# Kernel tuning notes

Hardware: AMD Instinct MI355X
Metric: run time of the kernel (lower is better)

## Reference

```python
import jax, jax.numpy as jnp
import numpy as np

HIDDEN_NF = 256
ATOMICA_DIM = 512
NUM_HEADS = 4
HEAD_DIM = HIDDEN_NF // NUM_HEADS
EDGE_CUTOFF = 10.0
N_LIG = 1024
N_POCKET = 8192
BOX = 30.0  # Angstrom box so the cutoff mask is selective


def _lin(key, fan_in, fan_out):
    kw, kb = jax.random.split(key)
    s = 1.0 / np.sqrt(fan_in)
    W = jax.random.uniform(kw, (fan_in, fan_out), jnp.float32, -s, s)
    b = jax.random.uniform(kb, (fan_out,), jnp.float32, -s, s)
    return W, b


def setup_inputs() -> dict:
    key = jax.random.key(0)
    ks = jax.random.split(key, 12)
    h_lig = jax.random.normal(ks[0], (N_LIG, HIDDEN_NF), jnp.float32)
    x_lig = jax.random.uniform(ks[1], (N_LIG, 3), jnp.float32) * BOX
    h_atomica = jax.random.normal(ks[2], (N_POCKET, ATOMICA_DIM), jnp.float32)
    x_pocket = jax.random.uniform(ks[3], (N_POCKET, 3), jnp.float32) * BOX
    qw, qb = _lin(ks[4], HIDDEN_NF, HIDDEN_NF)
    kw, kb = _lin(ks[5], ATOMICA_DIM, HIDDEN_NF)
    vw, vb = _lin(ks[6], ATOMICA_DIM, HIDDEN_NF)
    ow, ob = _lin(ks[7], HIDDEN_NF, HIDDEN_NF)
    e1w, e1b = _lin(ks[8], 1, HIDDEN_NF)
    e2w, e2b = _lin(ks[9], HIDDEN_NF, NUM_HEADS)
    c1w, c1b = _lin(ks[10], HIDDEN_NF, HIDDEN_NF)
    c2w, c2b = _lin(ks[11], HIDDEN_NF, 1)
    return dict(h_lig=h_lig, x_lig=x_lig, h_atomica=h_atomica, x_pocket=x_pocket,
                qw=qw, qb=qb, kw=kw, kb=kb, vw=vw, vb=vb, ow=ow, ob=ob,
                e1w=e1w, e1b=e1b, e2w=e2w, e2b=e2b,
                c1w=c1w, c1b=c1b, c2w=c2w, c2b=c2b)


def reference(h_lig, x_lig, h_atomica, x_pocket,
              qw, qb, kw, kb, vw, vb, ow, ob,
              e1w, e1b, e2w, e2b, c1w, c1b, c2w, c2b):
    N_lig = h_lig.shape[0]
    silu = jax.nn.silu
    # pairwise geometry: [N_lig, N_pocket, 3]
    rel_pos = x_pocket[None, :, :] - x_lig[:, None, :]
    distances = jnp.linalg.norm(rel_pos, axis=-1, keepdims=True)  # [Nl,Np,1]
    # edge bias MLP: [Nl,Np,num_heads]
    edge_attr = silu(distances @ e1w + e1b) @ e2w + e2b
    mask = distances[..., 0] < EDGE_CUTOFF  # [Nl,Np]
    Q = (h_lig @ qw + qb).reshape(N_lig, NUM_HEADS, HEAD_DIM)
    K = (h_atomica @ kw + kb).reshape(-1, NUM_HEADS, HEAD_DIM)
    V = (h_atomica @ vw + vb).reshape(-1, NUM_HEADS, HEAD_DIM)
    scores = jnp.einsum('ihd,jhd->ijh', Q, K) / np.sqrt(HEAD_DIM).astype(np.float32)
    scores = scores + edge_attr
    scores = jnp.where(mask[..., None], scores, -jnp.inf)
    attn = jax.nn.softmax(scores, axis=1)
    attn = jnp.where(jnp.isnan(attn), 0.0, attn)  # nan_to_num for fully-masked rows
    h_attended = jnp.einsum('ijh,jhd->ihd', attn, V).reshape(N_lig, HIDDEN_NF)
    h_out = h_lig + h_attended @ ow + ob
    # equivariant coordinate update
    normalized_rel_pos = rel_pos / (distances + 1e-8)
    avg_attn = attn.mean(axis=-1, keepdims=True)  # [Nl,Np,1]
    coord_messages = (avg_attn * normalized_rel_pos).sum(axis=1)  # [Nl,3]
    coord_scale = silu(h_attended @ c1w + c1b) @ c2w + c2b  # [Nl,1]
    x_out = x_lig + coord_scale * coord_messages
    return h_out, x_out
```

## Files before the change

kernel.cpp:

```cpp
#include <hip/hip_runtime.h>
#include <hip/hip_bf16.h>


#define NLIG   1024
#define NPOCK  8192
#define HIDDEN 256
#define ADIM   512
#define NHEAD  4
#define HDIM   64
#define NTAB   1024
#define NSPLIT 16
#define CHUNK  (NPOCK / NSPLIT)
#define NT     (CHUNK / 32)
#define LOG2E  1.4426950408889634f
#define QK_SCALE (0.125f * LOG2E)

typedef float f32x16 __attribute__((ext_vector_type(16)));
typedef short short8 __attribute__((ext_vector_type(8)));

union U4S8 { uint4 u; short8 s; };

static __device__ __forceinline__ float exp2h(float x) {
  float r; asm("v_exp_f32 %0, %1" : "=v"(r) : "v"(x)); return r;
}
static __device__ __forceinline__ float rsqh(float x) {
  float r; asm("v_rsq_f32 %0, %1" : "=v"(r) : "v"(x)); return r;
}
static __device__ __forceinline__ unsigned cvtpk(float lo, float hi) {
  unsigned r;
  asm("v_cvt_pk_bf16_f32 %0, %1, %2" : "=v"(r) : "v"(lo), "v"(hi));
  return r;
}
static __device__ __forceinline__ unsigned short f2bf(float f) {
  union { __hip_bfloat16 h; unsigned short u; } c;
  c.h = __float2bfloat16(f);
  return c.u;
}
static __device__ __forceinline__ float bf2f(unsigned u16) {
  union { unsigned uu; float f; } c;
  c.uu = u16 << 16;
  return c.f;
}
static __device__ __forceinline__ short8 load_bf8(const unsigned short* p) {
  U4S8 t; t.u = *(const uint4*)p; return t.s;
}
static __device__ __forceinline__ f32x16 mfma32(short8 a, short8 b, f32x16 c) {
  return __builtin_amdgcn_mfma_f32_32x32x16_bf16(a, b, c, 0, 0, 0);
}

#define NCAST 4352
#define NTRANS 448
__global__ __launch_bounds__(256)
void prep_kernel(const float* __restrict__ hA, const float* __restrict__ hl,
                 const float* __restrict__ qw, const float* __restrict__ kw,
                 const float* __restrict__ vw, const float* __restrict__ ow,
                 const float* __restrict__ c1w,
                 const float* __restrict__ e1w, const float* __restrict__ e1b,
                 const float* __restrict__ e2w, const float* __restrict__ e2b,
                 unsigned short* __restrict__ hAb, unsigned short* __restrict__ hlb,
                 unsigned short* __restrict__ qwT, unsigned short* __restrict__ kwT,
                 unsigned short* __restrict__ vwT, unsigned short* __restrict__ owT,
                 unsigned short* __restrict__ c1wT, float* __restrict__ tabG) {
  int bx = blockIdx.x;
  int tid = threadIdx.x;
  if (bx < NCAST) {
    int id = bx * 256 + tid;
    const int nA4 = NPOCK * ADIM / 4;
    if (id < nA4) {
      float4 v = ((const float4*)hA)[id];
      ushort4 o; o.x = f2bf(v.x); o.y = f2bf(v.y); o.z = f2bf(v.z); o.w = f2bf(v.w);
      ((ushort4*)hAb)[id] = o;
    } else {
      int j = id - nA4;
      float4 v = ((const float4*)hl)[j];
      ushort4 o; o.x = f2bf(v.x); o.y = f2bf(v.y); o.z = f2bf(v.z); o.w = f2bf(v.w);
      ((ushort4*)hlb)[j] = o;
    }
  } else if (bx < NCAST + NTRANS) {
    int b = bx - NCAST;
    const float* src; unsigned short* dst; int K;
    if (b < 64)       { src = qw;  dst = qwT;  K = 256; }
    else if (b < 192) { src = kw;  dst = kwT;  K = 512; b -= 64; }
    else if (b < 320) { src = vw;  dst = vwT;  K = 512; b -= 192; }
    else if (b < 384) { src = ow;  dst = owT;  K = 256; b -= 320; }
    else              { src = c1w; dst = c1wT; K = 256; b -= 384; }
    int kt = K / 32;
    int k0 = (b % kt) * 32, n0 = (b / kt) * 32;
    __shared__ float tile[32][33];
    int tx = tid & 31, ty = tid >> 5;
#pragma unroll
    for (int r = 0; r < 4; ++r)
      tile[ty + 8 * r][tx] = src[(k0 + ty + 8 * r) * 256 + n0 + tx];
    __syncthreads();
#pragma unroll
    for (int r = 0; r < 4; ++r)
      dst[(n0 + ty + 8 * r) * K + k0 + tx] = f2bf(tile[tx][ty + 8 * r]);
  } else {
    int eb = bx - (NCAST + NTRANS);
    int w = tid >> 6, l = tid & 63;
    int entry = eb * 4 + w;
    float d = (entry + 0.5f) * (10.0f / NTAB);
    float a0 = 0.f, a1 = 0.f, a2 = 0.f, a3 = 0.f;
#pragma unroll
    for (int jj = 0; jj < 4; ++jj) {
      int j = l + jj * 64;
      float v = fmaf(d, e1w[j], e1b[j]);
      float s = v / (1.0f + __expf(-v));
      float4 w2 = ((const float4*)e2w)[j];
      a0 = fmaf(s, w2.x, a0);
      a1 = fmaf(s, w2.y, a1);
      a2 = fmaf(s, w2.z, a2);
      a3 = fmaf(s, w2.w, a3);
    }
#pragma unroll
    for (int m = 32; m >= 1; m >>= 1) {
      a0 += __shfl_xor(a0, m); a1 += __shfl_xor(a1, m);
      a2 += __shfl_xor(a2, m); a3 += __shfl_xor(a3, m);
    }
    if (l == 0) {
      tabG[0 * NTAB + entry] = (a0 + e2b[0]) * LOG2E;
      tabG[1 * NTAB + entry] = (a1 + e2b[1]) * LOG2E;
      tabG[2 * NTAB + entry] = (a2 + e2b[2]) * LOG2E;
      tabG[3 * NTAB + entry] = (a3 + e2b[3]) * LOG2E;
    }
  }
}

__global__ __launch_bounds__(256)
void proj_kernel(const unsigned short* __restrict__ hAb, const unsigned short* __restrict__ hlb,
                 const unsigned short* __restrict__ kwT, const unsigned short* __restrict__ vwT,
                 const unsigned short* __restrict__ qwT,
                 const float* __restrict__ kb, const float* __restrict__ vb,
                 const float* __restrict__ qb,
                 unsigned short* __restrict__ Kb, unsigned short* __restrict__ VTb,
                 unsigned short* __restrict__ Qb) {
  int tid = threadIdx.x;
  int w = tid >> 6, lane = tid & 63;
  int lo = lane & 31, hi = lane >> 5;
  int n0 = blockIdx.y * 32;
  int n = n0 + lo;
  if (blockIdx.x < 64) {
    int m0 = blockIdx.x * 128 + w * 32;
    const unsigned short* ap  = hAb + (size_t)(m0 + lo) * ADIM + hi * 8;
    const unsigned short* bkp = kwT + (size_t)n * ADIM + hi * 8;
    const unsigned short* bvp = vwT + (size_t)n * ADIM + hi * 8;
    f32x16 aK, aV;
#pragma unroll
    for (int i = 0; i < 16; ++i) { aK[i] = 0.f; aV[i] = 0.f; }
#pragma unroll 8
    for (int kk = 0; kk < ADIM / 16; ++kk) {
      short8 a  = load_bf8(ap + kk * 16);
      short8 bk = load_bf8(bkp + kk * 16);
      short8 bv = load_bf8(bvp + kk * 16);
      aK = mfma32(a, bk, aK);
      aV = mfma32(bv, a, aV);
    }
    float bnK = kb[n];
#pragma unroll
    for (int g = 0; g < 4; ++g) {
#pragma unroll
      for (int rr = 0; rr < 4; ++rr) {
        int r = g * 4 + rr;
        int row = g * 8 + hi * 4 + rr;
        Kb[(size_t)(m0 + row) * HIDDEN + n] = f2bf(aK[r] + bnK);
        int nv = n0 + row;
        VTb[(size_t)nv * NPOCK + m0 + lo] = f2bf(aV[r] + vb[nv]);
      }
    }
  } else {
    int m0 = (blockIdx.x - 64) * 128 + w * 32;
    const unsigned short* ap = hlb + (size_t)(m0 + lo) * HIDDEN + hi * 8;
    const unsigned short* bp = qwT + (size_t)n * HIDDEN + hi * 8;
    f32x16 acc;
#pragma unroll
    for (int i = 0; i < 16; ++i) acc[i] = 0.f;
#pragma unroll 8
    for (int kk = 0; kk < HIDDEN / 16; ++kk) {
      short8 a = load_bf8(ap + kk * 16);
      short8 b = load_bf8(bp + kk * 16);
      acc = mfma32(a, b, acc);
    }
    float bn = qb[n];
#pragma unroll
    for (int g = 0; g < 4; ++g) {
#pragma unroll
      for (int rr = 0; rr < 4; ++rr) {
        int r = g * 4 + rr;
        int m = m0 + g * 8 + hi * 4 + rr;
        Qb[(size_t)m * HIDDEN + n] = f2bf(acc[r] + bn);
      }
    }
  }
}

__global__ __launch_bounds__(256)
void attn_kernel(const unsigned short* __restrict__ Qbf, const unsigned short* __restrict__ Kbf,
                 const unsigned short* __restrict__ VTbf,
                 const float* __restrict__ x_lig, const float* __restrict__ x_pocket,
                 const float* __restrict__ tabG,
                 unsigned* __restrict__ partOb, float4* __restrict__ partZC) {
  __shared__ float4 xch[CHUNK];
  __shared__ float tab[NHEAD][NTAB];

  int tid = threadIdx.x;
  int h = tid >> 6;
  int lane = tid & 63;
  int lo = lane & 31, hi = lane >> 5;
  int qt = blockIdx.x & 31;
  int split = blockIdx.x >> 5;
  int q0 = qt * 32;
  int j0g = split * CHUNK;

  for (int i = tid; i < CHUNK; i += 256) {
    float x = x_pocket[(j0g + i) * 3 + 0];
    float y = x_pocket[(j0g + i) * 3 + 1];
    float z = x_pocket[(j0g + i) * 3 + 2];
    float4 v; v.x = x; v.y = y; v.z = z; v.w = 0.f;
    xch[i] = v;
  }
  for (int i = tid; i < NHEAD * NTAB; i += 256) ((float*)tab)[i] = tabG[i];
  __syncthreads();

  int q = q0 + lo;
  float xl0 = x_lig[q * 3 + 0];
  float xl1 = x_lig[q * 3 + 1];
  float xl2 = x_lig[q * 3 + 2];

  short8 qfr[4];
#pragma unroll
  for (int kk = 0; kk < 4; ++kk)
    qfr[kk] = load_bf8(Qbf + (size_t)q * HIDDEN + h * HDIM + kk * 16 + hi * 8);

  const unsigned short* kbp = Kbf + (size_t)(j0g + lo) * HIDDEN + h * HDIM + hi * 8;
  const unsigned short* vbp = VTbf + (size_t)(h * HDIM + lo) * NPOCK + j0g + hi * 8;

  f32x16 O0, O1;
#pragma unroll
  for (int i = 0; i < 16; ++i) { O0[i] = 0.f; O1[i] = 0.f; }
  float Z = 0.f, c0 = 0.f, c1 = 0.f, c2 = 0.f;

  short8 kcur[4];
#pragma unroll
  for (int kk = 0; kk < 4; ++kk) kcur[kk] = load_bf8(kbp + kk * 16);

#pragma unroll 1
  for (int t = 0; t < NT; ++t) {
    int jb = t * 32;
    int tn = (t + 1 < NT) ? (t + 1) : t;
    short8 knx0 = load_bf8(kbp + (size_t)tn * 32 * HIDDEN + 0 * 16);
    short8 knx1 = load_bf8(kbp + (size_t)tn * 32 * HIDDEN + 1 * 16);
    short8 knx2 = load_bf8(kbp + (size_t)tn * 32 * HIDDEN + 2 * 16);
    short8 knx3 = load_bf8(kbp + (size_t)tn * 32 * HIDDEN + 3 * 16);
    short8 v00 = load_bf8(vbp + jb);
    short8 v01 = load_bf8(vbp + jb + (size_t)32 * NPOCK);
    short8 v10 = load_bf8(vbp + jb + 16);
    short8 v11 = load_bf8(vbp + jb + 16 + (size_t)32 * NPOCK);

    f32x16 s;
#pragma unroll
    for (int i = 0; i < 16; ++i) s[i] = 0.f;
    s = mfma32(kcur[0], qfr[0], s);
    s = mfma32(kcur[1], qfr[1], s);
    s = mfma32(kcur[2], qfr[2], s);
    s = mfma32(kcur[3], qfr[3], s);

    unsigned wp[8];
    float pprev = 0.f;
#pragma unroll
    for (int r = 0; r < 16; ++r) {
      int jl = (r & 3) + 8 * (r >> 2) + 4 * hi;
      float4 xp = xch[jb + jl];
      float dx = xp.x - xl0, dy = xp.y - xl1, dz = xp.z - xl2;
      float r2 = fmaf(dx, dx, fmaf(dy, dy, dz * dz));
      float r2c = fmaxf(r2, 1e-24f);
      float rinv = rsqh(r2c);
      float d = r2c * rinv;
      int idx = (int)(d * (NTAB / 10.0f));
      idx = idx > (NTAB - 1) ? (NTAB - 1) : idx;
      float b = tab[h][idx];
      float s2 = fmaf(s[r], QK_SCALE, b);
      float pe = (r2 < 100.0f) ? exp2h(s2) : 0.0f;
      Z += pe;
      float pr = pe * rinv;
      c0 = fmaf(pr, dx, c0);
      c1 = fmaf(pr, dy, c1);
      c2 = fmaf(pr, dz, c2);
      if (r & 1) wp[r >> 1] = cvtpk(pprev, pe); else pprev = pe;
    }
    {
      unsigned W0 = wp[0], W1 = wp[1], W2 = wp[2], W3 = wp[3];
      unsigned e01 = (unsigned)__shfl_xor((int)(hi ? W0 : W2), 32);
      unsigned e23 = (unsigned)__shfl_xor((int)(hi ? W1 : W3), 32);
      U4S8 pb;
      pb.u.x = hi ? e01 : W0;
      pb.u.y = hi ? e23 : W1;
      pb.u.z = hi ? W2 : e01;
      pb.u.w = hi ? W3 : e23;
      O0 = mfma32(v00, pb.s, O0);
      O1 = mfma32(v01, pb.s, O1);
    }
    {
      unsigned W0 = wp[4], W1 = wp[5], W2 = wp[6], W3 = wp[7];
      unsigned e01 = (unsigned)__shfl_xor((int)(hi ? W0 : W2), 32);
      unsigned e23 = (unsigned)__shfl_xor((int)(hi ? W1 : W3), 32);
      U4S8 pb;
      pb.u.x = hi ? e01 : W0;
      pb.u.y = hi ? e23 : W1;
      pb.u.z = hi ? W2 : e01;
      pb.u.w = hi ? W3 : e23;
      O0 = mfma32(v10, pb.s, O0);
      O1 = mfma32(v11, pb.s, O1);
    }
    kcur[0] = knx0; kcur[1] = knx1; kcur[2] = knx2; kcur[3] = knx3;
  }

  unsigned* po = partOb + (size_t)(((q * NHEAD) + h) * NSPLIT + split) * (HDIM / 2);
#pragma unroll
  for (int g = 0; g < 4; ++g) {
    uint2 u0;
    u0.x = cvtpk(O0[g * 4 + 0], O0[g * 4 + 1]);
    u0.y = cvtpk(O0[g * 4 + 2], O0[g * 4 + 3]);
    *(uint2*)(po + (g * 8 + hi * 4) / 2) = u0;
    uint2 u1;
    u1.x = cvtpk(O1[g * 4 + 0], O1[g * 4 + 1]);
    u1.y = cvtpk(O1[g * 4 + 2], O1[g * 4 + 3]);
    *(uint2*)(po + (32 + g * 8 + hi * 4) / 2) = u1;
  }
  float Zt = Z + __shfl_xor(Z, 32);
  float c0t = c0 + __shfl_xor(c0, 32);
  float c1t = c1 + __shfl_xor(c1, 32);
  float c2t = c2 + __shfl_xor(c2, 32);
  if (hi == 0) {
    float4 zc; zc.x = Zt; zc.y = c0t; zc.z = c1t; zc.w = c2t;
    partZC[((q * NHEAD) + h) * NSPLIT + split] = zc;
  }
}

__global__ __launch_bounds__(256)
void combine_kernel(const unsigned short* __restrict__ partOb, const float4* __restrict__ partZC,
                    unsigned short* __restrict__ hattb, float* __restrict__ cmsg) {
  int q = blockIdx.x;
  int t = threadIdx.x;
  int h = t >> 6, dl = t & 63;
  float Zh = 0.f;
#pragma unroll
  for (int s = 0; s < NSPLIT; ++s) Zh += partZC[(q * NHEAD + h) * NSPLIT + s].x;
  float o = 0.f;
#pragma unroll
  for (int s = 0; s < NSPLIT; ++s)
    o += bf2f(partOb[(size_t)((q * NHEAD + h) * NSPLIT + s) * HDIM + dl]);
  float inv = (Zh > 0.f) ? 1.0f / Zh : 0.f;
  hattb[(size_t)q * HIDDEN + h * HDIM + dl] = f2bf(o * inv);

  __shared__ float sm[NHEAD][3];
  if (t < NHEAD) {
    float zz = 0.f, a0 = 0.f, a1 = 0.f, a2 = 0.f;
    for (int s = 0; s < NSPLIT; ++s) {
      float4 v = partZC[(q * NHEAD + t) * NSPLIT + s];
      zz += v.x; a0 += v.y; a1 += v.z; a2 += v.w;
    }
    float iv = (zz > 0.f) ? 0.25f / zz : 0.f;
    sm[t][0] = a0 * iv; sm[t][1] = a1 * iv; sm[t][2] = a2 * iv;
  }
  __syncthreads();
  if (t < 3) cmsg[q * 3 + t] = sm[0][t] + sm[1][t] + sm[2][t] + sm[3][t];
}

__global__ __launch_bounds__(256)
void epi_kernel(const unsigned short* __restrict__ hatt,
                const unsigned short* __restrict__ owT, const unsigned short* __restrict__ c1wT,
                const float* __restrict__ ob, const float* __restrict__ c1b,
                const float* __restrict__ c2w, const float* __restrict__ h_lig,
                float* __restrict__ hout, float* __restrict__ cscale) {
  int tid = threadIdx.x;
  int w = tid >> 6, lane = tid & 63;
  int lo = lane & 31, hi = lane >> 5;
  int m0 = blockIdx.x * 128 + w * 32;
  int n0 = blockIdx.y * 32;
  int n = n0 + lo;
  const unsigned short* ap = hatt + (size_t)(m0 + lo) * HIDDEN + hi * 8;
  const unsigned short* bo = owT + (size_t)n * HIDDEN + hi * 8;
  const unsigned short* bc = c1wT + (size_t)n * HIDDEN + hi * 8;
  f32x16 aO, aC;
#pragma unroll
  for (int i = 0; i < 16; ++i) { aO[i] = 0.f; aC[i] = 0.f; }
#pragma unroll 8
  for (int kk = 0; kk < HIDDEN / 16; ++kk) {
    short8 a  = load_bf8(ap + kk * 16);
    short8 b1 = load_bf8(bo + kk * 16);
    short8 b2 = load_bf8(bc + kk * 16);
    aO = mfma32(a, b1, aO);
    aC = mfma32(a, b2, aC);
  }
  float obn = ob[n], c1bn = c1b[n], c2wn = c2w[n];
#pragma unroll
  for (int g = 0; g < 4; ++g) {
#pragma unroll
    for (int rr = 0; rr < 4; ++rr) {
      int r = g * 4 + rr;
      int m = m0 + g * 8 + hi * 4 + rr;
      hout[(size_t)m * HIDDEN + n] = aO[r] + obn + h_lig[(size_t)m * HIDDEN + n];
      float v = aC[r] + c1bn;
      float sg = v / (1.0f + exp2h(-LOG2E * v));
      float part = sg * c2wn;
#pragma unroll
      for (int msk = 16; msk >= 1; msk >>= 1) part += __shfl_xor(part, msk);
      if (lo == 0) atomicAdd(&cscale[m], part);
    }
  }
}

__global__ __launch_bounds__(256)
void coordfin_kernel(const float* __restrict__ cscale, const float* __restrict__ c2b,
                     const float* __restrict__ cmsg, const float* __restrict__ x_lig,
                     float* __restrict__ x_out) {
  int id = blockIdx.x * 256 + threadIdx.x;
  if (id < NLIG * 3) {
    int q = id / 3;
    x_out[id] = x_lig[id] + (cscale[q] + c2b[0]) * cmsg[id];
  }
}

extern "C" void kernel_launch(void* const* d_in, const int* in_sizes, int n_in,
                              void* d_out, int out_size, void* d_ws, size_t ws_size,
                              hipStream_t stream) {
  const float* h_lig  = (const float*)d_in[0];
  const float* x_lig  = (const float*)d_in[1];
  const float* h_atom = (const float*)d_in[2];
  const float* x_pock = (const float*)d_in[3];
  const float* qw  = (const float*)d_in[4];
  const float* qb  = (const float*)d_in[5];
  const float* kw  = (const float*)d_in[6];
  const float* kb  = (const float*)d_in[7];
  const float* vw  = (const float*)d_in[8];
  const float* vb  = (const float*)d_in[9];
  const float* ow  = (const float*)d_in[10];
  const float* ob  = (const float*)d_in[11];
  const float* e1w = (const float*)d_in[12];
  const float* e1b = (const float*)d_in[13];
  const float* e2w = (const float*)d_in[14];
  const float* e2b = (const float*)d_in[15];
  const float* c1w = (const float*)d_in[16];
  const float* c1b = (const float*)d_in[17];
  const float* c2w = (const float*)d_in[18];
  const float* c2b = (const float*)d_in[19];

  char* w = (char*)d_ws;
  unsigned short* hAb  = (unsigned short*)w; w += (size_t)NPOCK * ADIM * 2;
  unsigned short* hlb  = (unsigned short*)w; w += (size_t)NLIG * HIDDEN * 2;
  unsigned short* qwT  = (unsigned short*)w; w += 256 * 256 * 2;
  unsigned short* kwT  = (unsigned short*)w; w += 256 * 512 * 2;
  unsigned short* vwT  = (unsigned short*)w; w += 256 * 512 * 2;
  unsigned short* owT  = (unsigned short*)w; w += 256 * 256 * 2;
  unsigned short* c1wT = (unsigned short*)w; w += 256 * 256 * 2;
  unsigned short* Qb   = (unsigned short*)w; w += (size_t)NLIG * HIDDEN * 2;
  unsigned short* Kb   = (unsigned short*)w; w += (size_t)NPOCK * HIDDEN * 2;
  unsigned short* VTb  = (unsigned short*)w; w += (size_t)HIDDEN * NPOCK * 2;
  float* tabG          = (float*)w;          w += NHEAD * NTAB * 4;
  unsigned* partOb     = (unsigned*)w;       w += (size_t)NLIG * NHEAD * NSPLIT * HDIM * 2;
  float* partZC        = (float*)w;          w += (size_t)NLIG * NHEAD * NSPLIT * 4 * 4;
  unsigned short* hatt = (unsigned short*)w; w += (size_t)NLIG * HIDDEN * 2;
  float* cmsg          = (float*)w;          w += (size_t)NLIG * 3 * 4;
  float* cscale        = (float*)w;          w += (size_t)NLIG * 4;

  float* hout = (float*)d_out;
  float* xout = ((float*)d_out) + (size_t)NLIG * HIDDEN;

  prep_kernel<<<NCAST + NTRANS + NTAB / 4, 256, 0, stream>>>(
      h_atom, h_lig, qw, kw, vw, ow, c1w, e1w, e1b, e2w, e2b,
      hAb, hlb, qwT, kwT, vwT, owT, c1wT, tabG);
  proj_kernel<<<dim3(72, 8), 256, 0, stream>>>(
      hAb, hlb, kwT, vwT, qwT, kb, vb, qb, Kb, VTb, Qb);
  attn_kernel<<<32 * NSPLIT, 256, 0, stream>>>(Qb, Kb, VTb, x_lig, x_pock, tabG,
                                               partOb, (float4*)partZC);
  combine_kernel<<<NLIG, 256, 0, stream>>>((const unsigned short*)partOb,
                                           (const float4*)partZC, hatt, cmsg);
  hipMemsetAsync(cscale, 0, NLIG * sizeof(float), stream);
  epi_kernel<<<dim3(8, 8), 256, 0, stream>>>(hatt, owT, c1wT, ob, c1b, c2w, h_lig,
                                             hout, cscale);
  coordfin_kernel<<<(NLIG * 3 + 255) / 256, 256, 0, stream>>>(cscale, c2b, cmsg,
                                                              x_lig, xout);
}
```

Baseline: 208.7 us.

## Store bf16 operands in 32-row x 8-col tiled layout for coalesced MFMA loads

Introduces a tiled layout (t8) in which each 32-row by 8-column block is stored contiguously, so that the 64 lanes of an MFMA fragment load read one contiguous 512-byte span. The layout is applied to all bf16 intermediates (hA, h_lig, the transposed weights, Q, K, V^T, h_attended), and every producer and consumer is updated to match. It also reorders the split-partial buffers to a [split][q][...] layout so the combine kernel reads contiguously. The cost targeted is uncoalesced strided row loads. The prep and projection stores become more scattered as a result.

```diff
diff --git a/kernel.cpp b/kernel.cpp
--- a/kernel.cpp
+++ b/kernel.cpp
@@ -46,6 +46,9 @@
 }
 static __device__ __forceinline__ f32x16 mfma32(short8 a, short8 b, f32x16 c) {
   return __builtin_amdgcn_mfma_f32_32x32x16_bf16(a, b, c, 0, 0, 0);
+}
+static __device__ __forceinline__ size_t t8(int r, int c, int Cdiv8) {
+  return ((size_t)((r >> 5) * Cdiv8 + (c >> 3)) << 8) + ((r & 31) << 3) + (c & 7);
 }
 
 #define NCAST 4352
@@ -68,13 +71,15 @@
     const int nA4 = NPOCK * ADIM / 4;
     if (id < nA4) {
       float4 v = ((const float4*)hA)[id];
+      int r = id >> 7, c0 = (id << 2) & 511;
       ushort4 o; o.x = f2bf(v.x); o.y = f2bf(v.y); o.z = f2bf(v.z); o.w = f2bf(v.w);
-      ((ushort4*)hAb)[id] = o;
+      *(ushort4*)(hAb + t8(r, c0, 64)) = o;
     } else {
       int j = id - nA4;
       float4 v = ((const float4*)hl)[j];
+      int r = j >> 6, c0 = (j << 2) & 255;
       ushort4 o; o.x = f2bf(v.x); o.y = f2bf(v.y); o.z = f2bf(v.z); o.w = f2bf(v.w);
-      ((ushort4*)hlb)[j] = o;
+      *(ushort4*)(hlb + t8(r, c0, 32)) = o;
     }
   } else if (bx < NCAST + NTRANS) {
     int b = bx - NCAST;
@@ -94,7 +99,7 @@
     __syncthreads();
 #pragma unroll
     for (int r = 0; r < 4; ++r)
-      dst[(n0 + ty + 8 * r) * K + k0 + tx] = f2bf(tile[tx][ty + 8 * r]);
+      dst[t8(n0 + ty + 8 * r, k0 + tx, K >> 3)] = f2bf(tile[tx][ty + 8 * r]);
   } else {
     int eb = bx - (NCAST + NTRANS);
     int w = tid >> 6, l = tid & 63;
@@ -141,17 +146,17 @@
   int n = n0 + lo;
   if (blockIdx.x < 64) {
     int m0 = blockIdx.x * 128 + w * 32;
-    const unsigned short* ap  = hAb + (size_t)(m0 + lo) * ADIM + hi * 8;
-    const unsigned short* bkp = kwT + (size_t)n * ADIM + hi * 8;
-    const unsigned short* bvp = vwT + (size_t)n * ADIM + hi * 8;
+    const unsigned short* ap  = hAb + t8(m0 + lo, hi * 8, 64);
+    const unsigned short* bkp = kwT + t8(n, hi * 8, 64);
+    const unsigned short* bvp = vwT + t8(n, hi * 8, 64);
     f32x16 aK, aV;
 #pragma unroll
     for (int i = 0; i < 16; ++i) { aK[i] = 0.f; aV[i] = 0.f; }
 #pragma unroll 8
     for (int kk = 0; kk < ADIM / 16; ++kk) {
-      short8 a  = load_bf8(ap + kk * 16);
-      short8 bk = load_bf8(bkp + kk * 16);
-      short8 bv = load_bf8(bvp + kk * 16);
+      short8 a  = load_bf8(ap + kk * 512);
+      short8 bk = load_bf8(bkp + kk * 512);
+      short8 bv = load_bf8(bvp + kk * 512);
       aK = mfma32(a, bk, aK);
       aV = mfma32(bv, a, aV);
     }
@@ -162,22 +167,22 @@
       for (int rr = 0; rr < 4; ++rr) {
         int r = g * 4 + rr;
         int row = g * 8 + hi * 4 + rr;
-        Kb[(size_t)(m0 + row) * HIDDEN + n] = f2bf(aK[r] + bnK);
+        Kb[t8(m0 + row, n, 32)] = f2bf(aK[r] + bnK);
         int nv = n0 + row;
-        VTb[(size_t)nv * NPOCK + m0 + lo] = f2bf(aV[r] + vb[nv]);
+        VTb[t8(nv, m0 + lo, 1024)] = f2bf(aV[r] + vb[nv]);
       }
     }
   } else {
     int m0 = (blockIdx.x - 64) * 128 + w * 32;
-    const unsigned short* ap = hlb + (size_t)(m0 + lo) * HIDDEN + hi * 8;
-    const unsigned short* bp = qwT + (size_t)n * HIDDEN + hi * 8;
+    const unsigned short* ap = hlb + t8(m0 + lo, hi * 8, 32);
+    const unsigned short* bp = qwT + t8(n, hi * 8, 32);
     f32x16 acc;
 #pragma unroll
     for (int i = 0; i < 16; ++i) acc[i] = 0.f;
 #pragma unroll 8
     for (int kk = 0; kk < HIDDEN / 16; ++kk) {
-      short8 a = load_bf8(ap + kk * 16);
-      short8 b = load_bf8(bp + kk * 16);
+      short8 a = load_bf8(ap + kk * 512);
+      short8 b = load_bf8(bp + kk * 512);
       acc = mfma32(a, b, acc);
     }
     float bn = qb[n];
@@ -187,7 +192,7 @@
       for (int rr = 0; rr < 4; ++rr) {
         int r = g * 4 + rr;
         int m = m0 + g * 8 + hi * 4 + rr;
-        Qb[(size_t)m * HIDDEN + n] = f2bf(acc[r] + bn);
+        Qb[t8(m, n, 32)] = f2bf(acc[r] + bn);
       }
     }
   }
@@ -229,10 +234,10 @@
   short8 qfr[4];
 #pragma unroll
   for (int kk = 0; kk < 4; ++kk)
-    qfr[kk] = load_bf8(Qbf + (size_t)q * HIDDEN + h * HDIM + kk * 16 + hi * 8);
-
-  const unsigned short* kbp = Kbf + (size_t)(j0g + lo) * HIDDEN + h * HDIM + hi * 8;
-  const unsigned short* vbp = VTbf + (size_t)(h * HDIM + lo) * NPOCK + j0g + hi * 8;
+    qfr[kk] = load_bf8(Qbf + t8(q, h * HDIM + kk * 16 + hi * 8, 32));
+
+  const unsigned short* kbp = Kbf + t8(j0g + lo, h * HDIM + hi * 8, 32);
+  const unsigned short* vbp = VTbf + t8(h * HDIM + lo, j0g + hi * 8, 1024);
 
   f32x16 O0, O1;
 #pragma unroll
@@ -241,20 +246,20 @@
 
   short8 kcur[4];
 #pragma unroll
-  for (int kk = 0; kk < 4; ++kk) kcur[kk] = load_bf8(kbp + kk * 16);
+  for (int kk = 0; kk < 4; ++kk) kcur[kk] = load_bf8(kbp + kk * 512);
 
 #pragma unroll 1
   for (int t = 0; t < NT; ++t) {
     int jb = t * 32;
     int tn = (t + 1 < NT) ? (t + 1) : t;
-    short8 knx0 = load_bf8(kbp + (size_t)tn * 32 * HIDDEN + 0 * 16);
-    short8 knx1 = load_bf8(kbp + (size_t)tn * 32 * HIDDEN + 1 * 16);
-    short8 knx2 = load_bf8(kbp + (size_t)tn * 32 * HIDDEN + 2 * 16);
-    short8 knx3 = load_bf8(kbp + (size_t)tn * 32 * HIDDEN + 3 * 16);
-    short8 v00 = load_bf8(vbp + jb);
-    short8 v01 = load_bf8(vbp + jb + (size_t)32 * NPOCK);
-    short8 v10 = load_bf8(vbp + jb + 16);
-    short8 v11 = load_bf8(vbp + jb + 16 + (size_t)32 * NPOCK);
+    short8 knx0 = load_bf8(kbp + (size_t)tn * 8192 + 0 * 512);
+    short8 knx1 = load_bf8(kbp + (size_t)tn * 8192 + 1 * 512);
+    short8 knx2 = load_bf8(kbp + (size_t)tn * 8192 + 2 * 512);
+    short8 knx3 = load_bf8(kbp + (size_t)tn * 8192 + 3 * 512);
+    short8 v00 = load_bf8(vbp + (size_t)t * 1024);
+    short8 v01 = load_bf8(vbp + (size_t)t * 1024 + 262144);
+    short8 v10 = load_bf8(vbp + (size_t)t * 1024 + 512);
+    short8 v11 = load_bf8(vbp + (size_t)t * 1024 + 512 + 262144);
 
     f32x16 s;
 #pragma unroll
@@ -314,17 +319,17 @@
     kcur[0] = knx0; kcur[1] = knx1; kcur[2] = knx2; kcur[3] = knx3;
   }
 
-  unsigned* po = partOb + (size_t)(((q * NHEAD) + h) * NSPLIT + split) * (HDIM / 2);
+  unsigned* po = partOb + ((size_t)(split * NLIG + q) * (HIDDEN / 2)) + h * (HDIM / 2);
 #pragma unroll
   for (int g = 0; g < 4; ++g) {
     uint2 u0;
     u0.x = cvtpk(O0[g * 4 + 0], O0[g * 4 + 1]);
     u0.y = cvtpk(O0[g * 4 + 2], O0[g * 4 + 3]);
-    *(uint2*)(po + (g * 8 + hi * 4) / 2) = u0;
+    *(uint2*)(po + g * 4 + hi * 2) = u0;
     uint2 u1;
     u1.x = cvtpk(O1[g * 4 + 0], O1[g * 4 + 1]);
     u1.y = cvtpk(O1[g * 4 + 2], O1[g * 4 + 3]);
-    *(uint2*)(po + (32 + g * 8 + hi * 4) / 2) = u1;
+    *(uint2*)(po + 16 + g * 4 + hi * 2) = u1;
   }
   float Zt = Z + __shfl_xor(Z, 32);
   float c0t = c0 + __shfl_xor(c0, 32);
@@ -332,7 +337,7 @@
   float c2t = c2 + __shfl_xor(c2, 32);
   if (hi == 0) {
     float4 zc; zc.x = Zt; zc.y = c0t; zc.z = c1t; zc.w = c2t;
-    partZC[((q * NHEAD) + h) * NSPLIT + split] = zc;
+    partZC[(size_t)(split * NLIG + q) * NHEAD + h] = zc;
   }
 }
 
@@ -341,22 +346,22 @@
                     unsigned short* __restrict__ hattb, float* __restrict__ cmsg) {
   int q = blockIdx.x;
   int t = threadIdx.x;
-  int h = t >> 6, dl = t & 63;
+  int h = t >> 6;
   float Zh = 0.f;
 #pragma unroll
-  for (int s = 0; s < NSPLIT; ++s) Zh += partZC[(q * NHEAD + h) * NSPLIT + s].x;
+  for (int s = 0; s < NSPLIT; ++s) Zh += partZC[(size_t)(s * NLIG + q) * NHEAD + h].x;
   float o = 0.f;
 #pragma unroll
   for (int s = 0; s < NSPLIT; ++s)
-    o += bf2f(partOb[(size_t)((q * NHEAD + h) * NSPLIT + s) * HDIM + dl]);
+    o += bf2f(partOb[(size_t)(s * NLIG + q) * HIDDEN + t]);
   float inv = (Zh > 0.f) ? 1.0f / Zh : 0.f;
-  hattb[(size_t)q * HIDDEN + h * HDIM + dl] = f2bf(o * inv);
+  hattb[t8(q, t, 32)] = f2bf(o * inv);
 
   __shared__ float sm[NHEAD][3];
   if (t < NHEAD) {
     float zz = 0.f, a0 = 0.f, a1 = 0.f, a2 = 0.f;
     for (int s = 0; s < NSPLIT; ++s) {
-      float4 v = partZC[(q * NHEAD + t) * NSPLIT + s];
+      float4 v = partZC[(size_t)(s * NLIG + q) * NHEAD + t];
       zz += v.x; a0 += v.y; a1 += v.z; a2 += v.w;
     }
     float iv = (zz > 0.f) ? 0.25f / zz : 0.f;
@@ -378,17 +383,17 @@
   int m0 = blockIdx.x * 128 + w * 32;
   int n0 = blockIdx.y * 32;
   int n = n0 + lo;
-  const unsigned short* ap = hatt + (size_t)(m0 + lo) * HIDDEN + hi * 8;
-  const unsigned short* bo = owT + (size_t)n * HIDDEN + hi * 8;
-  const unsigned short* bc = c1wT + (size_t)n * HIDDEN + hi * 8;
+  const unsigned short* ap = hatt + t8(m0 + lo, hi * 8, 32);
+  const unsigned short* bo = owT + t8(n, hi * 8, 32);
+  const unsigned short* bc = c1wT + t8(n, hi * 8, 32);
   f32x16 aO, aC;
 #pragma unroll
   for (int i = 0; i < 16; ++i) { aO[i] = 0.f; aC[i] = 0.f; }
 #pragma unroll 8
   for (int kk = 0; kk < HIDDEN / 16; ++kk) {
-    short8 a  = load_bf8(ap + kk * 16);
-    short8 b1 = load_bf8(bo + kk * 16);
-    short8 b2 = load_bf8(bc + kk * 16);
+    short8 a  = load_bf8(ap + kk * 512);
+    short8 b1 = load_bf8(bo + kk * 512);
+    short8 b2 = load_bf8(bc + kk * 512);
     aO = mfma32(a, b1, aO);
     aC = mfma32(a, b2, aC);
   }
@@ -457,8 +462,8 @@
   unsigned short* Kb   = (unsigned short*)w; w += (size_t)NPOCK * HIDDEN * 2;
   unsigned short* VTb  = (unsigned short*)w; w += (size_t)HIDDEN * NPOCK * 2;
   float* tabG          = (float*)w;          w += NHEAD * NTAB * 4;
-  unsigned* partOb     = (unsigned*)w;       w += (size_t)NLIG * NHEAD * NSPLIT * HDIM * 2;
-  float* partZC        = (float*)w;          w += (size_t)NLIG * NHEAD * NSPLIT * 4 * 4;
+  unsigned* partOb     = (unsigned*)w;       w += (size_t)NSPLIT * NLIG * HIDDEN * 2;
+  float* partZC        = (float*)w;          w += (size_t)NSPLIT * NLIG * NHEAD * 4 * 4;
   unsigned short* hatt = (unsigned short*)w; w += (size_t)NLIG * HIDDEN * 2;
   float* cmsg          = (float*)w;          w += (size_t)NLIG * 3 * 4;
   float* cscale        = (float*)w;          w += (size_t)NLIG * 4;
```

After: 182.7 us. 12.4% less time.
